# Optimization experiments

Measured on AMD Instinct MI355X. Metric: run time of the kernel, lower is better.

## Reference

```python
import jax, jax.numpy as jnp
import numpy as np

N, E, NODE_DIM, EDGE_DIM, H, L, G, C = 50000, 600000, 64, 16, 128, 3, 256, 2


def setup_inputs() -> dict:
    key = jax.random.key(0)
    ks = jax.random.split(key, 32)
    inp = {
        "x": jax.random.normal(ks[0], (N, NODE_DIM), jnp.float32),
        "edge_attr": jax.random.normal(ks[1], (E, EDGE_DIM), jnp.float32),
        "edge_index": jax.random.randint(ks[2], (2, E), 0, N, dtype=jnp.int64),
        "batch": jnp.sort(jax.random.randint(ks[3], (N,), 0, G, dtype=jnp.int64)),
    }
    def lin(k, fan_in, fan_out):
        b = 1.0 / np.sqrt(fan_in)
        return jax.random.uniform(k, (fan_in, fan_out), jnp.float32, -b, b)
    # node embedding
    inp["emb_W"] = lin(ks[4], NODE_DIM, H)
    inp["emb_b"] = jnp.zeros((H,), jnp.float32)
    # stacked per-layer MPNN params [L, ...]
    inp["msg_W1"] = jnp.stack([lin(jax.random.fold_in(ks[5], i), 2 * H + EDGE_DIM, H) for i in range(L)])
    inp["msg_b1"] = jnp.zeros((L, H), jnp.float32)
    inp["msg_W2"] = jnp.stack([lin(jax.random.fold_in(ks[6], i), H, H) for i in range(L)])
    inp["msg_b2"] = jnp.zeros((L, H), jnp.float32)
    inp["upd_W1"] = jnp.stack([lin(jax.random.fold_in(ks[7], i), 2 * H, H) for i in range(L)])
    inp["upd_b1"] = jnp.zeros((L, H), jnp.float32)
    inp["upd_W2"] = jnp.stack([lin(jax.random.fold_in(ks[8], i), H, H) for i in range(L)])
    inp["upd_b2"] = jnp.zeros((L, H), jnp.float32)
    # classifier (dropout is eval-mode identity)
    inp["cls_W1"] = lin(ks[9], 2 * H, H)
    inp["cls_b1"] = jnp.zeros((H,), jnp.float32)
    inp["cls_W2"] = lin(ks[10], H, H // 2)
    inp["cls_b2"] = jnp.zeros((H // 2,), jnp.float32)
    inp["cls_W3"] = lin(ks[11], H // 2, C)
    inp["cls_b3"] = jnp.zeros((C,), jnp.float32)
    return inp


def reference(x, edge_attr, emb_W, emb_b, msg_W1, msg_b1, msg_W2, msg_b2,
              upd_W1, upd_b1, upd_W2, upd_b2,
              cls_W1, cls_b1, cls_W2, cls_b2, cls_W3, cls_b3,
              edge_index, batch):
    src, dst = edge_index[0], edge_index[1]  # PyG: x_j = x[src], x_i = x[dst]
    h = x @ emb_W + emb_b  # [N, H]
    for l in range(L):
        x_i = h[dst]
        x_j = h[src]
        msg_in = jnp.concatenate([x_i, x_j, edge_attr], axis=1)  # [E, 2H+edge_dim]
        m = jax.nn.relu(msg_in @ msg_W1[l] + msg_b1[l]) @ msg_W2[l] + msg_b2[l]
        aggr = jax.ops.segment_sum(m, dst, num_segments=N)  # scatter-add to targets
        upd_in = jnp.concatenate([h, aggr], axis=1)  # [N, 2H]
        h = jax.nn.relu(upd_in @ upd_W1[l] + upd_b1[l]) @ upd_W2[l] + upd_b2[l]
        h = jax.nn.relu(h)
    # global mean / max pool over graphs
    counts = jax.ops.segment_sum(jnp.ones((N,), h.dtype), batch, num_segments=G)
    g_mean = jax.ops.segment_sum(h, batch, num_segments=G) / jnp.maximum(counts, 1.0)[:, None]
    g_max = jax.ops.segment_max(h, batch, num_segments=G)
    g_max = jnp.where(jnp.isfinite(g_max), g_max, 0.0)  # guard empty graphs
    rep = jnp.concatenate([g_mean, g_max], axis=1)  # [G, 2H]
    # classifier (dropout = identity in eval)
    z = jax.nn.relu(rep @ cls_W1 + cls_b1)
    z = jax.nn.relu(z @ cls_W2 + cls_b2)
    return z @ cls_W3 + cls_b3  # [G, C]
```

## Files before the change

### kernel.cpp

```cpp
#include <hip/hip_runtime.h>
#include <hip/hip_bf16.h>

#define HD 128
#define SCB 2048

typedef __attribute__((ext_vector_type(8))) short short8v;
typedef __attribute__((ext_vector_type(4))) float f32x4;
typedef unsigned short us;

__device__ __forceinline__ us f2bf(float f) {
    union { float f; unsigned u; } c; c.f = f;
    unsigned u = c.u;
    return (us)((u + 0x7fffu + ((u >> 16) & 1u)) >> 16);
}
__device__ __forceinline__ float bf2f(us b) {
    union { unsigned u; float f; } c; c.u = ((unsigned)b) << 16;
    return c.f;
}

template<int KSTEPS, int K1S, bool HASA2, bool RELU, bool DEGB, bool WF32, bool WBF>
__global__ __launch_bounds__(512) void k_mgemm(
    const us* __restrict__ A1h, const us* __restrict__ A1l,
    const us* __restrict__ A2h, const us* __restrict__ A2l,
    const us* __restrict__ Wth, const us* __restrict__ Wtl,
    const float* __restrict__ bias,
    const float* __restrict__ bdeg, const float* __restrict__ deg,
    float* __restrict__ Cf0, float* __restrict__ Cf1,
    us* __restrict__ Ch, us* __restrict__ Cl,
    int nrows)
{
    constexpr int K   = KSTEPS * 32;
    constexpr int CPR = K / 8;
    constexpr int ITER = (64 * CPR) / 512;
    __shared__ us As_h[64 * K];
    __shared__ us As_l[64 * K];

    const int tid  = threadIdx.x;
    const int wv   = tid >> 6;
    const int lane = tid & 63;
    const int r    = lane & 15;
    const int g    = lane >> 4;
    const int rb   = blockIdx.x * 64;
    const int col  = blockIdx.y * 128 + wv * 16 + r;

    short8v bh[KSTEPS], bl[KSTEPS];
    {
        size_t wbase = (size_t)col * K + (size_t)(g * 8);
#pragma unroll
        for (int s = 0; s < KSTEPS; ++s) {
            bh[s] = *(const short8v*)(Wth + wbase + s * 32);
            bl[s] = *(const short8v*)(Wtl + wbase + s * 32);
        }
    }

#pragma unroll
    for (int i = 0; i < ITER; ++i) {
        int f = tid + i * 512;
        int row = f / CPR, c = f % CPR;
        int grow = rb + row; if (grow >= nrows) grow = nrows - 1;
        uint4 vh, vl;
        if (!HASA2 || c * 8 < K1S) {
            size_t o = (size_t)grow * K1S + (size_t)(c * 8);
            vh = *(const uint4*)(A1h + o);
            vl = *(const uint4*)(A1l + o);
        } else {
            size_t o = (size_t)grow * (K - K1S) + (size_t)(c * 8 - K1S);
            vh = *(const uint4*)(A2h + o);
            vl = *(const uint4*)(A2l + o);
        }
        int boff = row * (K * 2) + ((c * 16) ^ ((row & 7) << 4));
        *(uint4*)((char*)As_h + boff) = vh;
        *(uint4*)((char*)As_l + boff) = vl;
    }
    __syncthreads();

    f32x4 acc[4];
#pragma unroll
    for (int t = 0; t < 4; ++t) acc[t] = (f32x4){0.f, 0.f, 0.f, 0.f};

#pragma unroll
    for (int s = 0; s < KSTEPS; ++s) {
#pragma unroll
        for (int t = 0; t < 4; ++t) {
            int row = t * 16 + r;
            int boff = row * (K * 2) + (((s * 64) + g * 16) ^ ((row & 7) << 4));
            short8v ah = *(const short8v*)((const char*)As_h + boff);
            short8v al = *(const short8v*)((const char*)As_l + boff);
            acc[t] = __builtin_amdgcn_mfma_f32_16x16x32_bf16(ah, bh[s], acc[t], 0, 0, 0);
            acc[t] = __builtin_amdgcn_mfma_f32_16x16x32_bf16(al, bh[s], acc[t], 0, 0, 0);
            acc[t] = __builtin_amdgcn_mfma_f32_16x16x32_bf16(ah, bl[s], acc[t], 0, 0, 0);
        }
    }

    const float bb = (bias && col < 128) ? bias[col] : 0.f;
    const float bd = (DEGB && col < 128) ? bdeg[col] : 0.f;
    const int jc = col & 127;
#pragma unroll
    for (int t = 0; t < 4; ++t) {
#pragma unroll
        for (int i = 0; i < 4; ++i) {
            int row = rb + t * 16 + g * 4 + i;
            if (row >= nrows) continue;
            float v = acc[t][i] + bb;
            if (DEGB) v += deg[row] * bd;
            if (RELU) v = fmaxf(v, 0.f);
            size_t o = (size_t)row * HD + jc;
            if (WF32) (col < 128 ? Cf0 : Cf1)[o] = v;
            if (WBF) {
                us hh = f2bf(v);
                Ch[o] = hh;
                Cl[o] = f2bf(v - bf2f(hh));
            }
        }
    }
}

__global__ void k_cvtA(const float* __restrict__ src,
                       us* __restrict__ dh, us* __restrict__ dl, long n)
{
    long i = (long)blockIdx.x * blockDim.x + threadIdx.x;
    if (i >= n) return;
    float v = src[i];
    us h = f2bf(v);
    dh[i] = h;
    dl[i] = f2bf(v - bf2f(h));
}

__global__ void k_cvtW(const float* __restrict__ src, long sstride, int K,
                       us* __restrict__ dh, us* __restrict__ dl, long dstride)
{
    int l = blockIdx.y;
    int idx = blockIdx.x * 256 + threadIdx.x;
    if (idx >= K * 128) return;
    int k = idx >> 7, j = idx & 127;
    float v = src[(size_t)l * sstride + (size_t)k * 128 + j];
    us h = f2bf(v);
    size_t o = (size_t)l * dstride + (size_t)j * K + k;
    dh[o] = h;
    dl[o] = f2bf(v - bf2f(h));
}

__global__ void k_cvtW2(const float* __restrict__ srcA, long strideA,
                        const float* __restrict__ srcB, long strideB,
                        int K1s, int K,
                        us* __restrict__ dh, us* __restrict__ dl, long dstride)
{
    int l = blockIdx.y;
    int idx = blockIdx.x * 256 + threadIdx.x;
    if (idx >= K * 128) return;
    int k = idx >> 7, j = idx & 127;
    float v = (k < K1s)
        ? srcA[(size_t)l * strideA + (size_t)k * 128 + j]
        : srcB[(size_t)l * strideB + (size_t)(k - K1s) * 128 + j];
    us h = f2bf(v);
    size_t o = (size_t)l * dstride + (size_t)j * K + k;
    dh[o] = h;
    dl[o] = f2bf(v - bf2f(h));
}

__global__ void k_deghist(const int* __restrict__ dst, int* __restrict__ degi, int E,
                          const int* __restrict__ batch, int* __restrict__ gcnt, int N)
{
    int i = blockIdx.x * blockDim.x + threadIdx.x;
    if (i < E) atomicAdd(&degi[dst[i]], 1);
    if (i < N) atomicAdd(&gcnt[batch[i]], 1);
}

__global__ __launch_bounds__(256) void k_scan1(const int* __restrict__ degi,
                                               int* __restrict__ thrpre,
                                               int* __restrict__ bsum, int N)
{
    __shared__ int sc[256];
    const int t = threadIdx.x, b = blockIdx.x;
    int i0 = b * SCB + t * 8;
    int s = 0;
#pragma unroll
    for (int q = 0; q < 8; ++q) {
        int i = i0 + q;
        if (i < N) s += degi[i];
    }
    sc[t] = s;
    __syncthreads();
    for (int o = 1; o < 256; o <<= 1) {
        int v = (t >= o) ? sc[t - o] : 0;
        __syncthreads();
        sc[t] += v;
        __syncthreads();
    }
    thrpre[b * 256 + t] = sc[t] - s;
    if (t == 255) bsum[b] = sc[255];
}

__global__ void k_scan2(const int* __restrict__ bsum, int* __restrict__ boff, int nb)
{
    if (threadIdx.x == 0 && blockIdx.x == 0) {
        int run = 0;
        for (int b = 0; b < nb; ++b) { boff[b] = run; run += bsum[b]; }
    }
}

__global__ __launch_bounds__(256) void k_scan3(
    const int* __restrict__ degi, const int* __restrict__ thrpre,
    const int* __restrict__ boff,
    int* __restrict__ rowptr, int* __restrict__ cursor,
    float* __restrict__ degf, int N, int E)
{
    const int t = threadIdx.x, b = blockIdx.x;
    int run = boff[b] + thrpre[b * 256 + t];
    int i0 = b * SCB + t * 8;
#pragma unroll
    for (int q = 0; q < 8; ++q) {
        int i = i0 + q;
        if (i < N) {
            int d = degi[i];
            rowptr[i] = run;
            cursor[i] = run;
            degf[i] = (float)d;
            run += d;
        }
    }
    if (b == 0 && t == 0) rowptr[N] = E;
}

__global__ void k_scatter(const int* __restrict__ dst, const int* __restrict__ src,
                          int* __restrict__ cursor,
                          const float* __restrict__ ea,
                          int* __restrict__ csr_src, int* __restrict__ csr_eid,
                          float* __restrict__ ea_p, int E)
{
    int e = blockIdx.x * blockDim.x + threadIdx.x;
    if (e >= E) return;
    int d = dst[e];
    int pos = atomicAdd(&cursor[d], 1);
    csr_src[pos] = src[e];
    if (ea_p) {
        const float4* s4 = (const float4*)&ea[(size_t)e * 16];
        float4* d4 = (float4*)&ea_p[(size_t)pos * 16];
        d4[0] = s4[0]; d4[1] = s4[1]; d4[2] = s4[2]; d4[3] = s4[3];
    } else {
        csr_eid[pos] = e;
    }
}

__global__ __launch_bounds__(256) void k_foldW(
    const float* __restrict__ msg_W2, const float* __restrict__ upd_W1,
    float* __restrict__ fold)
{
    int l = blockIdx.x >> 3, rb = blockIdx.x & 7;
    const float* W2  = msg_W2 + (size_t)l * HD * HD;
    const float* U1b = upd_W1 + (size_t)l * 256 * HD + (size_t)HD * HD;
    float* Wout = fold + (size_t)l * HD * HD;
    int j = threadIdx.x & 127;
    int rh = threadIdx.x >> 7;
    int r0 = rb * 16 + rh * 8;
    float acc[8] = {0.f,0.f,0.f,0.f,0.f,0.f,0.f,0.f};
    for (int k = 0; k < HD; ++k) {
        float u = U1b[(size_t)k * HD + j];
#pragma unroll
        for (int rr = 0; rr < 8; ++rr)
            acc[rr] = fmaf(W2[(size_t)(r0 + rr) * HD + k], u, acc[rr]);
    }
#pragma unroll
    for (int rr = 0; rr < 8; ++rr)
        Wout[(size_t)(r0 + rr) * HD + j] = acc[rr];
}

__global__ __launch_bounds__(128) void k_foldb(
    const float* __restrict__ msg_b2, const float* __restrict__ upd_W1,
    float* __restrict__ bvec2)
{
    int l = blockIdx.x, j = threadIdx.x;
    const float* U1b = upd_W1 + (size_t)l * 256 * HD + (size_t)HD * HD;
    const float* b2 = msg_b2 + (size_t)l * HD;
    float acc = 0.f;
    for (int k = 0; k < HD; ++k) acc = fmaf(b2[k], U1b[(size_t)k * HD + j], acc);
    bvec2[(size_t)l * HD + j] = acc;
}

#define EB 16
template<bool PERM>
__global__ __launch_bounds__(256) void k_edge(
    const float* __restrict__ P, const float* __restrict__ Q,
    const float* __restrict__ EA,
    const int* __restrict__ rowptr,
    const int* __restrict__ csr_src, const int* __restrict__ csr_eid,
    const float* __restrict__ W1c,
    us* __restrict__ Sh, us* __restrict__ Sl, int N)
{
    const int lane = threadIdx.x & 63;
    const int node = __builtin_amdgcn_readfirstlane(blockIdx.x * 4 + (threadIdx.x >> 6));
    if (node >= N) return;
    float wA[16], wB[16];
#pragma unroll
    for (int k = 0; k < 16; ++k) {
        wA[k] = W1c[k * HD + lane];
        wB[k] = W1c[k * HD + 64 + lane];
    }
    const int beg = __builtin_amdgcn_readfirstlane(rowptr[node]);
    const int end = __builtin_amdgcn_readfirstlane(rowptr[node + 1]);
    const float pA = P[(size_t)node * HD + lane];
    const float pB = P[(size_t)node * HD + 64 + lane];
    float accA = 0.f, accB = 0.f;

    for (int i = beg; i < end; i += EB) {
        int sv[EB], ei[EB];
#pragma unroll
        for (int r = 0; r < EB; ++r) {
            int ii = i + r; ii = (ii < end) ? ii : (end - 1);
            ei[r] = PERM ? ii : __builtin_amdgcn_readfirstlane(csr_eid[ii]);
            sv[r] = __builtin_amdgcn_readfirstlane(csr_src[ii]);
        }
        float qA[EB], qB[EB];
#pragma unroll
        for (int r = 0; r < EB; ++r) {
            qA[r] = Q[(size_t)sv[r] * HD + lane];
            qB[r] = Q[(size_t)sv[r] * HD + 64 + lane];
        }
#pragma unroll
        for (int r = 0; r < EB; ++r) {
            const float4* Ev = (const float4*)&EA[(size_t)ei[r] * 16];
            float4 v0 = Ev[0], v1 = Ev[1], v2 = Ev[2], v3 = Ev[3];
            float tA = pA + qA[r], tB = pB + qB[r];
            tA = fmaf(v0.x, wA[0],  tA); tB = fmaf(v0.x, wB[0],  tB);
            tA = fmaf(v0.y, wA[1],  tA); tB = fmaf(v0.y, wB[1],  tB);
            tA = fmaf(v0.z, wA[2],  tA); tB = fmaf(v0.z, wB[2],  tB);
            tA = fmaf(v0.w, wA[3],  tA); tB = fmaf(v0.w, wB[3],  tB);
            tA = fmaf(v1.x, wA[4],  tA); tB = fmaf(v1.x, wB[4],  tB);
            tA = fmaf(v1.y, wA[5],  tA); tB = fmaf(v1.y, wB[5],  tB);
            tA = fmaf(v1.z, wA[6],  tA); tB = fmaf(v1.z, wB[6],  tB);
            tA = fmaf(v1.w, wA[7],  tA); tB = fmaf(v1.w, wB[7],  tB);
            tA = fmaf(v2.x, wA[8],  tA); tB = fmaf(v2.x, wB[8],  tB);
            tA = fmaf(v2.y, wA[9],  tA); tB = fmaf(v2.y, wB[9],  tB);
            tA = fmaf(v2.z, wA[10], tA); tB = fmaf(v2.z, wB[10], tB);
            tA = fmaf(v2.w, wA[11], tA); tB = fmaf(v2.w, wB[11], tB);
            tA = fmaf(v3.x, wA[12], tA); tB = fmaf(v3.x, wB[12], tB);
            tA = fmaf(v3.y, wA[13], tA); tB = fmaf(v3.y, wB[13], tB);
            tA = fmaf(v3.z, wA[14], tA); tB = fmaf(v3.z, wB[14], tB);
            tA = fmaf(v3.w, wA[15], tA); tB = fmaf(v3.w, wB[15], tB);
            bool ok = (i + r) < end;
            accA += ok ? fmaxf(tA, 0.f) : 0.f;
            accB += ok ? fmaxf(tB, 0.f) : 0.f;
        }
    }
    size_t oA = (size_t)node * HD + lane;
    size_t oB = oA + 64;
    us hA = f2bf(accA);
    us hB = f2bf(accB);
    Sh[oA] = hA; Sl[oA] = f2bf(accA - bf2f(hA));
    Sh[oB] = hB; Sl[oB] = f2bf(accB - bf2f(hB));
}

__global__ __launch_bounds__(256) void k_pool2(
    const us* __restrict__ hh, const us* __restrict__ hl,
    const int* __restrict__ batch,
    float* __restrict__ gsum, unsigned int* __restrict__ gmax, int N)
{
    int nchunk = (N + gridDim.x - 1) / gridDim.x;
    int n0 = blockIdx.x * nchunk;
    int n1 = n0 + nchunk; if (n1 > N) n1 = N;
    int j = threadIdx.x & 127;
    int half = threadIdx.x >> 7;
    float s = 0.f, m = 0.f; int gcur = -1;
    for (int n = n0 + half; n < n1; n += 2) {
        int g = batch[n];
        if (g != gcur) {
            if (gcur >= 0) {
                atomicAdd(&gsum[(size_t)gcur * HD + j], s);
                atomicMax(&gmax[(size_t)gcur * HD + j], __float_as_uint(m));
            }
            gcur = g; s = 0.f; m = 0.f;
        }
        size_t o = (size_t)n * HD + j;
        float v = bf2f(hh[o]) + bf2f(hl[o]);
        s += v; m = fmaxf(m, v);
    }
    if (gcur >= 0) {
        atomicAdd(&gsum[(size_t)gcur * HD + j], s);
        atomicMax(&gmax[(size_t)gcur * HD + j], __float_as_uint(m));
    }
}

__global__ __launch_bounds__(128) void k_cls(
    const float* __restrict__ gsum, const float* __restrict__ gmax,
    const int* __restrict__ gcnt,
    const float* __restrict__ W1, const float* __restrict__ b1,
    const float* __restrict__ W2, const float* __restrict__ b2,
    const float* __restrict__ W3, const float* __restrict__ b3,
    float* __restrict__ out)
{
    __shared__ float rep[256];
    __shared__ float z1[128];
    __shared__ float z2[64];
    const int g = blockIdx.x;
    const int j = threadIdx.x;
    float cntf = (float)gcnt[g];
    rep[j]       = gsum[(size_t)g * HD + j] / fmaxf(cntf, 1.f);
    rep[128 + j] = gmax[(size_t)g * HD + j];
    __syncthreads();
    float a = 0.f;
    for (int k = 0; k < 256; ++k) a = fmaf(rep[k], W1[(size_t)k * 128 + j], a);
    z1[j] = fmaxf(a + b1[j], 0.f);
    __syncthreads();
    if (j < 64) {
        float b = 0.f;
        for (int k = 0; k < 128; ++k) b = fmaf(z1[k], W2[(size_t)k * 64 + j], b);
        z2[j] = fmaxf(b + b2[j], 0.f);
    }
    __syncthreads();
    if (j < 2) {
        float c = 0.f;
        for (int k = 0; k < 64; ++k) c = fmaf(z2[k], W3[(size_t)k * 2 + j], c);
        out[(size_t)g * 2 + j] = c + b3[j];
    }
}

extern "C" void kernel_launch(void* const* d_in, const int* in_sizes, int n_in,
                              void* d_out, int out_size, void* d_ws, size_t ws_size,
                              hipStream_t stream) {
    const float* x      = (const float*)d_in[0];
    const float* ea     = (const float*)d_in[1];
    const int*   ei     = (const int*)d_in[2];
    const int*   batch  = (const int*)d_in[3];
    const float* emb_W  = (const float*)d_in[4];
    const float* emb_b  = (const float*)d_in[5];
    const float* msg_W1 = (const float*)d_in[6];
    const float* msg_b1 = (const float*)d_in[7];
    const float* msg_W2 = (const float*)d_in[8];
    const float* msg_b2 = (const float*)d_in[9];
    const float* upd_W1 = (const float*)d_in[10];
    const float* upd_b1 = (const float*)d_in[11];
    const float* upd_W2 = (const float*)d_in[12];
    const float* upd_b2 = (const float*)d_in[13];
    const float* cW1 = (const float*)d_in[14];
    const float* cb1 = (const float*)d_in[15];
    const float* cW2 = (const float*)d_in[16];
    const float* cb2 = (const float*)d_in[17];
    const float* cW3 = (const float*)d_in[18];
    const float* cb3 = (const float*)d_in[19];

    const int N = in_sizes[0] / 64;
    const int E = in_sizes[1] / 16;
    const int G = 256, L = 3;
    const int* src = ei;
    const int* dst = ei + E;
    const int nb = (N + SCB - 1) / SCB;

    char* w = (char*)d_ws;
    size_t off = 0;
    auto alloc = [&](size_t bytes) -> void* {
        void* p = w + off;
        off += (bytes + 255) & ~(size_t)255;
        return p;
    };
    float* Pb  = (float*)alloc((size_t)N * HD * 4);
    float* Qb  = (float*)alloc((size_t)N * HD * 4);
    us* S_h = (us*)alloc((size_t)N * HD * 2);
    us* S_l = (us*)alloc((size_t)N * HD * 2);
    us* h_h = (us*)alloc((size_t)N * HD * 2);
    us* h_l = (us*)alloc((size_t)N * HD * 2);
    us* U_h = (us*)Pb;
    us* U_l = U_h + (size_t)N * HD;
    us* x_h = S_h;
    us* x_l = S_l;
    float* fold  = (float*)alloc((size_t)L * HD * HD * 4);
    float* bvec2 = (float*)alloc((size_t)L * HD * 4);
    us* embt_h = (us*)alloc((size_t)128 * 64 * 2);
    us* embt_l = (us*)alloc((size_t)128 * 64 * 2);
    us* WPQt_h = (us*)alloc((size_t)L * 256 * 128 * 2);
    us* WPQt_l = (us*)alloc((size_t)L * 256 * 128 * 2);
    us* Wcbt_h = (us*)alloc((size_t)L * 128 * 256 * 2);
    us* Wcbt_l = (us*)alloc((size_t)L * 128 * 256 * 2);
    us* U2t_h  = (us*)alloc((size_t)L * 128 * 128 * 2);
    us* U2t_l  = (us*)alloc((size_t)L * 128 * 128 * 2);
    int*   degi   = (int*)alloc((size_t)N * 4);
    float* degf   = (float*)alloc((size_t)N * 4);
    int*   rowptr = (int*)alloc((size_t)(N + 1) * 4);
    int*   cursor = (int*)alloc((size_t)N * 4);
    int*   thrpre = (int*)alloc((size_t)nb * 256 * 4);
    int*   bsum   = (int*)alloc((size_t)(nb + 1) * 4);
    int*   boff   = (int*)alloc((size_t)(nb + 1) * 4);
    int*   gcnt   = (int*)alloc(256 * 4);
    float* gsum   = (float*)alloc((size_t)G * HD * 4);
    float* gmax   = (float*)alloc((size_t)G * HD * 4);
    int*   csr_src = (int*)alloc((size_t)E * 4);
    int*   csr_eid = (int*)alloc((size_t)E * 4);
    float* ea_p = nullptr;
    if (ws_size && off + (size_t)E * 16 * 4 + 256 <= ws_size)
        ea_p = (float*)alloc((size_t)E * 16 * 4);
    (void)n_in; (void)out_size;

    hipMemsetAsync(degi, 0, (size_t)N * 4, stream);
    hipMemsetAsync(gcnt, 0, 256 * 4, stream);
    hipMemsetAsync(gsum, 0, (size_t)G * HD * 4, stream);
    hipMemsetAsync(gmax, 0, (size_t)G * HD * 4, stream);

    int mEN = (E > N ? E : N);
    k_deghist<<<(mEN + 255) / 256, 256, 0, stream>>>(dst, degi, E, batch, gcnt, N);
    k_scan1<<<nb, 256, 0, stream>>>(degi, thrpre, bsum, N);
    k_scan2<<<1, 64, 0, stream>>>(bsum, boff, nb);
    k_scan3<<<nb, 256, 0, stream>>>(degi, thrpre, boff, rowptr, cursor, degf, N, E);
    k_scatter<<<(E + 255) / 256, 256, 0, stream>>>(dst, src, cursor, ea,
                                                   csr_src, csr_eid, ea_p, E);

    k_foldW<<<L * 8, 256, 0, stream>>>(msg_W2, upd_W1, fold);
    k_foldb<<<L, 128, 0, stream>>>(msg_b2, upd_W1, bvec2);

    k_cvtA<<<(int)(((long)N * 64 + 255) / 256), 256, 0, stream>>>(x, x_h, x_l, (long)N * 64);
    k_cvtW<<<dim3(32, 1), 256, 0, stream>>>(emb_W, 0, 64, embt_h, embt_l, 0);
    k_cvtW<<<dim3(64, L), 256, 0, stream>>>(msg_W1, 272 * 128, 128,
                                            WPQt_h, WPQt_l, 256 * 128);
    k_cvtW<<<dim3(64, L), 256, 0, stream>>>(msg_W1 + 128 * 128, 272 * 128, 128,
                                            WPQt_h + 128 * 128, WPQt_l + 128 * 128,
                                            256 * 128);
    k_cvtW2<<<dim3(128, L), 256, 0, stream>>>(upd_W1, 256 * 128, fold, 128 * 128,
                                              128, 256, Wcbt_h, Wcbt_l, 128 * 256);
    k_cvtW<<<dim3(64, L), 256, 0, stream>>>(upd_W2, 128 * 128, 128,
                                            U2t_h, U2t_l, 128 * 128);

    const int gb = (N + 63) / 64;
    k_mgemm<2, 64, false, false, false, false, true><<<dim3(gb, 1), 512, 0, stream>>>(
        x_h, x_l, nullptr, nullptr, embt_h, embt_l,
        emb_b, nullptr, nullptr, nullptr, nullptr, h_h, h_l, N);

    for (int l = 0; l < L; ++l) {
        const float* W1 = msg_W1 + (size_t)l * 272 * HD;
        k_mgemm<4, 128, false, false, false, true, false><<<dim3(gb, 2), 512, 0, stream>>>(
            h_h, h_l, nullptr, nullptr,
            WPQt_h + (size_t)l * 256 * 128, WPQt_l + (size_t)l * 256 * 128,
            msg_b1 + (size_t)l * HD, nullptr, nullptr, Pb, Qb, nullptr, nullptr, N);
        if (ea_p)
            k_edge<true><<<(N + 3) / 4, 256, 0, stream>>>(Pb, Qb, ea_p, rowptr,
                                                          csr_src, nullptr,
                                                          W1 + 256 * HD, S_h, S_l, N);
        else
            k_edge<false><<<(N + 3) / 4, 256, 0, stream>>>(Pb, Qb, ea, rowptr,
                                                           csr_src, csr_eid,
                                                           W1 + 256 * HD, S_h, S_l, N);
        k_mgemm<8, 128, true, true, true, false, true><<<dim3(gb, 1), 512, 0, stream>>>(
            h_h, h_l, S_h, S_l,
            Wcbt_h + (size_t)l * 128 * 256, Wcbt_l + (size_t)l * 128 * 256,
            upd_b1 + (size_t)l * HD, bvec2 + (size_t)l * HD, degf,
            nullptr, nullptr, U_h, U_l, N);
        k_mgemm<4, 128, false, true, false, false, true><<<dim3(gb, 1), 512, 0, stream>>>(
            U_h, U_l, nullptr, nullptr,
            U2t_h + (size_t)l * 128 * 128, U2t_l + (size_t)l * 128 * 128,
            upd_b2 + (size_t)l * HD, nullptr, nullptr, nullptr, nullptr, h_h, h_l, N);
    }

    k_pool2<<<1024, 256, 0, stream>>>(h_h, h_l, batch, gsum, (unsigned int*)gmax, N);
    k_cls<<<G, 128, 0, stream>>>(gsum, gmax, gcnt, cW1, cb1, cW2, cb2, cW3, cb3,
                                 (float*)d_out);
}
```

Baseline: 699.1 us.

## Fuse two update-MLP GEMMs into one kernel and batch CSR index loads

```diff
diff --git a/kernel.cpp b/kernel.cpp
--- a/kernel.cpp
+++ b/kernel.cpp
@@ -115,6 +115,144 @@
     }
 }
 
+__global__ __launch_bounds__(512) void k_upd(
+    const us* __restrict__ A1h, const us* __restrict__ A1l,
+    const us* __restrict__ A2h, const us* __restrict__ A2l,
+    const us* __restrict__ Wth, const us* __restrict__ Wtl,
+    const float* __restrict__ b1,
+    const float* __restrict__ bdeg, const float* __restrict__ deg,
+    const us* __restrict__ W2th, const us* __restrict__ W2tl,
+    const float* __restrict__ b2,
+    us* __restrict__ out_h, us* __restrict__ out_l,
+    int nrows)
+{
+    constexpr int K = 256;
+    constexpr int CPR = K / 8;
+    constexpr int ITER = (64 * CPR) / 512;
+    __shared__ us As_h[64 * K];
+    __shared__ us As_l[64 * K];
+
+    const int tid  = threadIdx.x;
+    const int wv   = tid >> 6;
+    const int lane = tid & 63;
+    const int r    = lane & 15;
+    const int g    = lane >> 4;
+    const int rb   = blockIdx.x * 64;
+    const int col  = wv * 16 + r;
+
+    short8v bh[8], bl[8];
+    {
+        size_t wbase = (size_t)col * K + (size_t)(g * 8);
+#pragma unroll
+        for (int s = 0; s < 8; ++s) {
+            bh[s] = *(const short8v*)(Wth + wbase + s * 32);
+            bl[s] = *(const short8v*)(Wtl + wbase + s * 32);
+        }
+    }
+
+#pragma unroll
+    for (int i = 0; i < ITER; ++i) {
+        int f = tid + i * 512;
+        int row = f / CPR, c = f % CPR;
+        int grow = rb + row; if (grow >= nrows) grow = nrows - 1;
+        uint4 vh, vl;
+        if (c * 8 < 128) {
+            size_t o = (size_t)grow * 128 + (size_t)(c * 8);
+            vh = *(const uint4*)(A1h + o);
+            vl = *(const uint4*)(A1l + o);
+        } else {
+            size_t o = (size_t)grow * 128 + (size_t)(c * 8 - 128);
+            vh = *(const uint4*)(A2h + o);
+            vl = *(const uint4*)(A2l + o);
+        }
+        int boff = row * (K * 2) + ((c * 16) ^ ((row & 7) << 4));
+        *(uint4*)((char*)As_h + boff) = vh;
+        *(uint4*)((char*)As_l + boff) = vl;
+    }
+    __syncthreads();
+
+    f32x4 acc[4];
+#pragma unroll
+    for (int t = 0; t < 4; ++t) acc[t] = (f32x4){0.f, 0.f, 0.f, 0.f};
+#pragma unroll
+    for (int s = 0; s < 8; ++s) {
+#pragma unroll
+        for (int t = 0; t < 4; ++t) {
+            int row = t * 16 + r;
+            int boff = row * (K * 2) + (((s * 64) + g * 16) ^ ((row & 7) << 4));
+            short8v ah = *(const short8v*)((const char*)As_h + boff);
+            short8v al = *(const short8v*)((const char*)As_l + boff);
+            acc[t] = __builtin_amdgcn_mfma_f32_16x16x32_bf16(ah, bh[s], acc[t], 0, 0, 0);
+            acc[t] = __builtin_amdgcn_mfma_f32_16x16x32_bf16(al, bh[s], acc[t], 0, 0, 0);
+            acc[t] = __builtin_amdgcn_mfma_f32_16x16x32_bf16(ah, bl[s], acc[t], 0, 0, 0);
+        }
+    }
+    __syncthreads();
+
+    short8v b2h[4], b2l[4];
+    {
+        size_t wbase = (size_t)col * 128 + (size_t)(g * 8);
+#pragma unroll
+        for (int s = 0; s < 4; ++s) {
+            b2h[s] = *(const short8v*)(W2th + wbase + s * 32);
+            b2l[s] = *(const short8v*)(W2tl + wbase + s * 32);
+        }
+    }
+
+    {
+        const float bb = b1[col];
+        const float bd = bdeg[col];
+#pragma unroll
+        for (int t = 0; t < 4; ++t) {
+#pragma unroll
+            for (int i = 0; i < 4; ++i) {
+                int lrow = t * 16 + g * 4 + i;
+                int grow = rb + lrow;
+                float dg = (grow < nrows) ? deg[grow] : 0.f;
+                float v = acc[t][i] + bb + dg * bd;
+                v = fmaxf(v, 0.f);
+                us uh = f2bf(v);
+                us ul = f2bf(v - bf2f(uh));
+                int byte = lrow * 256 + ((col * 2) ^ ((lrow & 7) << 4));
+                *(us*)((char*)As_h + byte) = uh;
+                *(us*)((char*)As_l + byte) = ul;
+            }
+        }
+    }
+    __syncthreads();
+
+    f32x4 acc2[4];
+#pragma unroll
+    for (int t = 0; t < 4; ++t) acc2[t] = (f32x4){0.f, 0.f, 0.f, 0.f};
+#pragma unroll
+    for (int s = 0; s < 4; ++s) {
+#pragma unroll
+        for (int t = 0; t < 4; ++t) {
+            int row = t * 16 + r;
+            int boff = row * 256 + (((s * 64) + g * 16) ^ ((row & 7) << 4));
+            short8v ah = *(const short8v*)((const char*)As_h + boff);
+            short8v al = *(const short8v*)((const char*)As_l + boff);
+            acc2[t] = __builtin_amdgcn_mfma_f32_16x16x32_bf16(ah, b2h[s], acc2[t], 0, 0, 0);
+            acc2[t] = __builtin_amdgcn_mfma_f32_16x16x32_bf16(al, b2h[s], acc2[t], 0, 0, 0);
+            acc2[t] = __builtin_amdgcn_mfma_f32_16x16x32_bf16(ah, b2l[s], acc2[t], 0, 0, 0);
+        }
+    }
+    const float bb2 = b2[col];
+#pragma unroll
+    for (int t = 0; t < 4; ++t) {
+#pragma unroll
+        for (int i = 0; i < 4; ++i) {
+            int row = rb + t * 16 + g * 4 + i;
+            if (row >= nrows) continue;
+            float v = fmaxf(acc2[t][i] + bb2, 0.f);
+            size_t o = (size_t)row * HD + col;
+            us hh = f2bf(v);
+            out_h[o] = hh;
+            out_l[o] = f2bf(v - bf2f(hh));
+        }
+    }
+}
+
 __global__ void k_cvtA(const float* __restrict__ src,
                        us* __restrict__ dh, us* __restrict__ dl, long n)
 {
@@ -303,12 +441,15 @@
     float accA = 0.f, accB = 0.f;
 
     for (int i = beg; i < end; i += EB) {
+        int myi = i + (lane & 15);
+        myi = (myi < end) ? myi : (end - 1);
+        int myidx = PERM ? myi : csr_eid[myi];
+        int mysrc = csr_src[myi];
         int sv[EB], ei[EB];
 #pragma unroll
         for (int r = 0; r < EB; ++r) {
-            int ii = i + r; ii = (ii < end) ? ii : (end - 1);
-            ei[r] = PERM ? ii : __builtin_amdgcn_readfirstlane(csr_eid[ii]);
-            sv[r] = __builtin_amdgcn_readfirstlane(csr_src[ii]);
+            sv[r] = __builtin_amdgcn_readlane(mysrc, r);
+            ei[r] = PERM ? 0 : __builtin_amdgcn_readlane(myidx, r);
         }
         float qA[EB], qB[EB];
 #pragma unroll
@@ -318,7 +459,9 @@
         }
 #pragma unroll
         for (int r = 0; r < EB; ++r) {
-            const float4* Ev = (const float4*)&EA[(size_t)ei[r] * 16];
+            int ii = i + r; ii = (ii < end) ? ii : (end - 1);
+            const float4* Ev = PERM ? (const float4*)&EA[(size_t)ii * 16]
+                                    : (const float4*)&EA[(size_t)ei[r] * 16];
             float4 v0 = Ev[0], v1 = Ev[1], v2 = Ev[2], v3 = Ev[3];
             float tA = pA + qA[r], tB = pB + qB[r];
             tA = fmaf(v0.x, wA[0],  tA); tB = fmaf(v0.x, wB[0],  tB);
@@ -458,8 +601,6 @@
     us* S_l = (us*)alloc((size_t)N * HD * 2);
     us* h_h = (us*)alloc((size_t)N * HD * 2);
     us* h_l = (us*)alloc((size_t)N * HD * 2);
-    us* U_h = (us*)Pb;
-    us* U_l = U_h + (size_t)N * HD;
     us* x_h = S_h;
     us* x_l = S_l;
     float* fold  = (float*)alloc((size_t)L * HD * HD * 4);
@@ -536,15 +677,13 @@
             k_edge<false><<<(N + 3) / 4, 256, 0, stream>>>(Pb, Qb, ea, rowptr,
                                                            csr_src, csr_eid,
                                                            W1 + 256 * HD, S_h, S_l, N);
-        k_mgemm<8, 128, true, true, true, false, true><<<dim3(gb, 1), 512, 0, stream>>>(
+        k_upd<<<gb, 512, 0, stream>>>(
             h_h, h_l, S_h, S_l,
             Wcbt_h + (size_t)l * 128 * 256, Wcbt_l + (size_t)l * 128 * 256,
             upd_b1 + (size_t)l * HD, bvec2 + (size_t)l * HD, degf,
-            nullptr, nullptr, U_h, U_l, N);
-        k_mgemm<4, 128, false, true, false, false, true><<<dim3(gb, 1), 512, 0, stream>>>(
-            U_h, U_l, nullptr, nullptr,
             U2t_h + (size_t)l * 128 * 128, U2t_l + (size_t)l * 128 * 128,
-            upd_b2 + (size_t)l * HD, nullptr, nullptr, nullptr, nullptr, h_h, h_l, N);
+            upd_b2 + (size_t)l * HD,
+            h_h, h_l, N);
     }
 
     k_pool2<<<1024, 256, 0, stream>>>(h_h, h_l, batch, gsum, (unsigned int*)gmax, N);
```

Result: no change. 688.9 us (-1.5%).
